# Performance work log

Measured on AMD Instinct MI355X. Metric: run time of the kernel, lower is better.

The kernel has to match this reference:

```python
import jax, jax.numpy as jnp
import numpy as np

N_NODES = 100000
N_EDGES = 1600000
D_IN = 256
N_HEADS = 4
D_OUT = 32
NEG_SLOPE = 0.2


def setup_inputs() -> dict:
    key = jax.random.key(0)
    k1, k2, k3, k4, k5, k6 = jax.random.split(key, 6)
    x = jax.random.normal(k1, (N_NODES, D_IN), dtype=jnp.float32)
    fc_w = jax.random.normal(k2, (N_HEADS * D_OUT, D_IN), dtype=jnp.float32) * (1.0 / np.sqrt(D_IN))
    attn_l = jax.random.normal(k3, (N_HEADS, D_OUT), dtype=jnp.float32) * 0.1
    attn_r = jax.random.normal(k4, (N_HEADS, D_OUT), dtype=jnp.float32) * 0.1
    src = jax.random.randint(k5, (N_EDGES,), 0, N_NODES, dtype=jnp.int64)
    dst = jax.random.randint(k6, (N_EDGES,), 0, N_NODES, dtype=jnp.int64)
    return {"x": x, "fc_w": fc_w, "attn_l": attn_l, "attn_r": attn_r, "src": src, "dst": dst}


def reference(x, fc_w, attn_l, attn_r, src, dst):
    N = x.shape[0]
    H, F = attn_l.shape
    # Linear projection: ft = fc(x) viewed as [N, H, F]
    ft = (x @ fc_w.T).reshape(N, H, F)
    # Per-node attention logits: el = <ft, a_l>, er = <ft, a_r>  -> [N, H]
    el = jnp.einsum("nhf,hf->nh", ft, attn_l)
    er = jnp.einsum("nhf,hf->nh", ft, attn_r)
    # Edge scores: e = leaky_relu(el[src] + er[dst])  -> [E, H]
    e = el[src] + er[dst]
    e = jnp.where(e > 0, e, NEG_SLOPE * e)
    # Segment (per-destination-node) softmax over incoming edges
    m = jax.ops.segment_max(e, dst, num_segments=N)  # [N, H]
    ex = jnp.exp(e - m[dst])                          # [E, H]
    denom = jax.ops.segment_sum(ex, dst, num_segments=N)  # [N, H]
    a = ex / denom[dst]                               # [E, H]
    # Weighted scatter-sum aggregation: out[n] = sum_{e: dst=n} a_e * ft[src_e]
    out = jax.ops.segment_sum(ft[src] * a[:, :, None], dst, num_segments=N)  # [N, H, F]
    return out
```

## Files before the change

### kernel.cpp

```cpp
#include <hip/hip_runtime.h>
#include <math.h>

#define N_NODES 100000
#define N_EDGES 1600000
#define D_IN 256
#define N_HEADS 4
#define D_OUT 32
#define D_HID 128
#define NEG_SLOPE 0.2f

#define BUCKET_SHIFT 8
#define BUCKET_NODES 256
#define NB ((N_NODES + BUCKET_NODES - 1) / BUCKET_NODES)
#define CAP 6144
#define TILE 2048
#define EPT 8
#define N_TILES ((N_EDGES + TILE - 1) / TILE)

typedef __attribute__((ext_vector_type(8))) short bf16x8;
typedef __attribute__((ext_vector_type(4))) float f32x4;

static __device__ __forceinline__ unsigned cvt2(float lo, float hi) {
  unsigned r;
  asm("v_cvt_pk_bf16_f32 %0, %1, %2" : "=v"(r) : "v"(lo), "v"(hi));
  return r;
}
static __device__ __forceinline__ float bfu_lo(unsigned u) {
  union { unsigned u; float f; } c; c.u = u << 16; return c.f;
}
static __device__ __forceinline__ float bfu_hi(unsigned u) {
  union { unsigned u; float f; } c; c.u = u & 0xFFFF0000u; return c.f;
}

#define LDA 40
__global__ __launch_bounds__(256) void k_gemm(const float* __restrict__ x,
                                              const float* __restrict__ w,
                                              const float* __restrict__ al,
                                              const float* __restrict__ ar,
                                              unsigned short* __restrict__ ftb,
                                              float* __restrict__ el,
                                              float* __restrict__ er) {
  __shared__ short As[128 * LDA];
  __shared__ short Bs[128 * LDA];
  int t = threadIdx.x;
  int wave = t >> 6, lane = t & 63;
  int quad = lane >> 4, l16 = lane & 15;
  int rowBase = blockIdx.x * 128;
  int wm = (wave >> 1) * 64, wn = (wave & 1) * 64;
  f32x4 acc[4][4];
  #pragma unroll
  for (int mt = 0; mt < 4; ++mt)
    #pragma unroll
    for (int nt = 0; nt < 4; ++nt) {
      acc[mt][nt][0] = 0.f; acc[mt][nt][1] = 0.f;
      acc[mt][nt][2] = 0.f; acc[mt][nt][3] = 0.f;
    }

  for (int kb = 0; kb < D_IN; kb += 32) {
    #pragma unroll
    for (int p = 0; p < 4; ++p) {
      int idx = p * 256 + t;
      int r = idx >> 3;
      int kq = (idx & 7) * 4;
      int row = rowBase + r;
      float4 v = make_float4(0.f, 0.f, 0.f, 0.f);
      if (row < N_NODES) v = *(const float4*)&x[(size_t)row * D_IN + kb + kq];
      unsigned* d = (unsigned*)&As[r * LDA + kq];
      d[0] = cvt2(v.x, v.y);
      d[1] = cvt2(v.z, v.w);
    }
    #pragma unroll
    for (int p = 0; p < 4; ++p) {
      int idx = p * 256 + t;
      int r = idx >> 3;
      int kq = (idx & 7) * 4;
      float4 v = *(const float4*)&w[(size_t)r * D_IN + kb + kq];
      unsigned* d = (unsigned*)&Bs[r * LDA + kq];
      d[0] = cvt2(v.x, v.y);
      d[1] = cvt2(v.z, v.w);
    }
    __syncthreads();
    bf16x8 af[4], bfr[4];
    #pragma unroll
    for (int mt = 0; mt < 4; ++mt)
      af[mt] = *(const bf16x8*)&As[(wm + mt * 16 + l16) * LDA + quad * 8];
    #pragma unroll
    for (int nt = 0; nt < 4; ++nt)
      bfr[nt] = *(const bf16x8*)&Bs[(wn + nt * 16 + l16) * LDA + quad * 8];
    #pragma unroll
    for (int mt = 0; mt < 4; ++mt)
      #pragma unroll
      for (int nt = 0; nt < 4; ++nt)
        acc[mt][nt] = __builtin_amdgcn_mfma_f32_16x16x32_bf16(af[mt], bfr[nt], acc[mt][nt], 0, 0, 0);
    __syncthreads();
  }

  #pragma unroll
  for (int mt = 0; mt < 4; ++mt) {
    #pragma unroll
    for (int nt = 0; nt < 4; ++nt) {
      int col = wn + nt * 16 + l16;
      #pragma unroll
      for (int r = 0; r < 4; r += 2) {
        unsigned p = cvt2(acc[mt][nt][r], acc[mt][nt][r + 1]);
        int row = rowBase + wm + mt * 16 + quad * 4 + r;
        if (row < N_NODES)
          ftb[(size_t)row * D_HID + col] = (unsigned short)p;
        if (row + 1 < N_NODES)
          ftb[(size_t)(row + 1) * D_HID + col] = (unsigned short)(p >> 16);
      }
    }
  }

  float alf[4], arf[4];
  #pragma unroll
  for (int q = 0; q < 4; ++q) {
    alf[q] = al[wn + q * 16 + l16];
    arf[q] = ar[wn + q * 16 + l16];
  }
  int h0 = wn >> 5;
  #pragma unroll
  for (int mt = 0; mt < 4; ++mt) {
    #pragma unroll
    for (int r = 0; r < 4; ++r) {
      float sl0 = acc[mt][0][r] * alf[0] + acc[mt][1][r] * alf[1];
      float sl1 = acc[mt][2][r] * alf[2] + acc[mt][3][r] * alf[3];
      float sr0 = acc[mt][0][r] * arf[0] + acc[mt][1][r] * arf[1];
      float sr1 = acc[mt][2][r] * arf[2] + acc[mt][3][r] * arf[3];
      #pragma unroll
      for (int o = 1; o < 16; o <<= 1) {
        sl0 += __shfl_xor(sl0, o);
        sl1 += __shfl_xor(sl1, o);
        sr0 += __shfl_xor(sr0, o);
        sr1 += __shfl_xor(sr1, o);
      }
      int row = rowBase + wm + mt * 16 + quad * 4 + r;
      if (l16 == 0 && row < N_NODES) {
        *(float2*)&el[row * 4 + h0] = make_float2(sl0, sl1);
        *(float2*)&er[row * 4 + h0] = make_float2(sr0, sr1);
      }
    }
  }
}

__global__ __launch_bounds__(256) void k_bucket(const int* __restrict__ src,
                                                const int* __restrict__ dst,
                                                int* __restrict__ gfill,
                                                unsigned* __restrict__ pairs,
                                                int* __restrict__ offs) {
  __shared__ int bcnt[NB];
  __shared__ int brsv[NB];
  __shared__ int brank[NB];
  int t = threadIdx.x;
  if (blockIdx.x == 0 && t == 0) offs[N_NODES] = N_EDGES;
  for (int tile = blockIdx.x; tile < N_TILES; tile += gridDim.x) {
    int e0 = tile * TILE + t * EPT;
    for (int i = t; i < NB; i += 256) { bcnt[i] = 0; brank[i] = 0; }
    __syncthreads();
    int ds[EPT], ss[EPT];
    if (e0 + EPT <= N_EDGES) {
      *(int4*)&ds[0] = *(const int4*)&dst[e0];
      *(int4*)&ds[4] = *(const int4*)&dst[e0 + 4];
      *(int4*)&ss[0] = *(const int4*)&src[e0];
      *(int4*)&ss[4] = *(const int4*)&src[e0 + 4];
    } else {
      #pragma unroll
      for (int k = 0; k < EPT; ++k) {
        int e = e0 + k;
        ds[k] = (e < N_EDGES) ? dst[e] : -1;
        ss[k] = (e < N_EDGES) ? src[e] : 0;
      }
    }
    #pragma unroll
    for (int k = 0; k < EPT; ++k)
      if (ds[k] >= 0) atomicAdd(&bcnt[ds[k] >> BUCKET_SHIFT], 1);
    __syncthreads();
    for (int i = t; i < NB; i += 256) {
      int c = bcnt[i];
      brsv[i] = (c > 0) ? atomicAdd(&gfill[i], c) : 0;
    }
    __syncthreads();
    #pragma unroll
    for (int k = 0; k < EPT; ++k) {
      if (ds[k] >= 0) {
        int b = ds[k] >> BUCKET_SHIFT;
        int r = brsv[b] + atomicAdd(&brank[b], 1);
        if (r < CAP)
          pairs[(size_t)b * CAP + r] =
              ((unsigned)ss[k] << 8) | (unsigned)(ds[k] & (BUCKET_NODES - 1));
      }
    }
    __syncthreads();
  }
}

__global__ __launch_bounds__(512) void k_localsort(const unsigned* __restrict__ pairs,
                                                   const int* __restrict__ gfill,
                                                   int* __restrict__ offs,
                                                   int* __restrict__ ssrc) {
  __shared__ int cnt_l[256];
  __shared__ int ss[256];
  __shared__ int cur_l[256];
  __shared__ int redsum[8];
  __shared__ int s_base;
  int b = blockIdx.x, t = threadIdx.x;
  {
    int v = (t < NB && t < b) ? gfill[t] : 0;
    #pragma unroll
    for (int o = 32; o > 0; o >>= 1) v += __shfl_xor(v, o);
    if ((t & 63) == 0) redsum[t >> 6] = v;
  }
  if (t < 256) cnt_l[t] = 0;
  __syncthreads();
  if (t == 0) {
    int s = 0;
    #pragma unroll
    for (int i = 0; i < 8; ++i) s += redsum[i];
    s_base = s;
  }
  int E = min(gfill[b], CAP);
  const unsigned* pb = &pairs[(size_t)b * CAP];
  __syncthreads();
  int base = s_base;
  for (int i = t; i < E; i += 512)
    atomicAdd(&cnt_l[pb[i] & (BUCKET_NODES - 1)], 1);
  __syncthreads();
  if (t < 256) ss[t] = cnt_l[t];
  __syncthreads();
  #pragma unroll
  for (int d = 1; d < 256; d <<= 1) {
    int u = (t < 256 && t >= d) ? ss[t - d] : 0;
    __syncthreads();
    if (t < 256) ss[t] += u;
    __syncthreads();
  }
  if (t < 256) {
    int pre = (t == 0) ? 0 : ss[t - 1];
    int node = b * BUCKET_NODES + t;
    if (node < N_NODES) offs[node] = base + pre;
    cur_l[t] = pre;
  }
  __syncthreads();
  for (int i = t; i < E; i += 512) {
    unsigned p = pb[i];
    int pos = atomicAdd(&cur_l[p & (BUCKET_NODES - 1)], 1);
    ssrc[base + pos] = (int)(p >> 8);
  }
}

#define AH_PAD 36
__global__ __launch_bounds__(256) void k_agg(const int* __restrict__ offs,
                                             const int* __restrict__ ssrc,
                                             const unsigned short* __restrict__ ftb,
                                             const float* __restrict__ el,
                                             const float* __restrict__ er,
                                             float* __restrict__ out) {
  __shared__ int   lds_s[4][2][32];
  __shared__ float lds_ah[4][2][4][AH_PAD];
  int wave = threadIdx.x >> 6;
  int lane = threadIdx.x & 63;
  int half = lane >> 5;
  int l32 = lane & 31;
  int n = blockIdx.x * 8 + wave * 2 + half;
  if (n >= N_NODES) return;
  int start = offs[n], end = offs[n + 1];
  int deg = end - start;

  int* sS = lds_s[wave][half];
  float (*sA)[AH_PAD] = lds_ah[wave][half];

  int c4 = l32 * 4;
  int hh = l32 >> 3;
  const unsigned short* fb = ftb + c4;
  float a0 = 0.f, a1 = 0.f, a2 = 0.f, a3 = 0.f;

  float4 er4 = *(const float4*)&er[n * 4];

  if (deg <= 32) {
    bool valid = l32 < deg;
    int s = valid ? ssrc[start + l32] : 0;
    float4 e4 = *(const float4*)&el[s * 4];
    float v[4] = {e4.x + er4.x, e4.y + er4.y, e4.z + er4.z, e4.w + er4.w};
    float m[4], ex[4], den[4];
    #pragma unroll
    for (int h = 0; h < 4; ++h) {
      v[h] = v[h] > 0.f ? v[h] : NEG_SLOPE * v[h];
      m[h] = valid ? v[h] : -INFINITY;
    }
    #pragma unroll
    for (int h = 0; h < 4; ++h)
      #pragma unroll
      for (int o = 16; o > 0; o >>= 1) m[h] = fmaxf(m[h], __shfl_xor(m[h], o));
    #pragma unroll
    for (int h = 0; h < 4; ++h) {
      ex[h] = valid ? __expf(v[h] - m[h]) : 0.f;
      den[h] = ex[h];
    }
    #pragma unroll
    for (int h = 0; h < 4; ++h)
      #pragma unroll
      for (int o = 16; o > 0; o >>= 1) den[h] += __shfl_xor(den[h], o);
    sS[l32] = s;
    #pragma unroll
    for (int h = 0; h < 4; ++h) sA[h][l32] = ex[h] / den[h];
    __builtin_amdgcn_wave_barrier();
    for (int j = 0; j < deg; j += 4) {
      int4   sv = *(const int4*)&sS[j];
      float4 av = *(const float4*)&sA[hh][j];
      uint2 uA = *(const uint2*)&fb[(size_t)sv.x * D_HID];
      uint2 uB = *(const uint2*)&fb[(size_t)sv.y * D_HID];
      uint2 uC = *(const uint2*)&fb[(size_t)sv.z * D_HID];
      uint2 uD = *(const uint2*)&fb[(size_t)sv.w * D_HID];
      a0 += av.x * bfu_lo(uA.x); a1 += av.x * bfu_hi(uA.x);
      a2 += av.x * bfu_lo(uA.y); a3 += av.x * bfu_hi(uA.y);
      a0 += av.y * bfu_lo(uB.x); a1 += av.y * bfu_hi(uB.x);
      a2 += av.y * bfu_lo(uB.y); a3 += av.y * bfu_hi(uB.y);
      a0 += av.z * bfu_lo(uC.x); a1 += av.z * bfu_hi(uC.x);
      a2 += av.z * bfu_lo(uC.y); a3 += av.z * bfu_hi(uC.y);
      a0 += av.w * bfu_lo(uD.x); a1 += av.w * bfu_hi(uD.x);
      a2 += av.w * bfu_lo(uD.y); a3 += av.w * bfu_hi(uD.y);
    }
  } else {
    float erh[4] = {er4.x, er4.y, er4.z, er4.w};
    float m[4] = {-INFINITY, -INFINITY, -INFINITY, -INFINITY};
    for (int c = start; c < end; c += 32) {
      int i = c + l32;
      bool valid = i < end;
      int s = valid ? ssrc[i] : 0;
      float4 e4 = *(const float4*)&el[s * 4];
      float ee[4] = {e4.x, e4.y, e4.z, e4.w};
      #pragma unroll
      for (int h = 0; h < 4; ++h) {
        float v = ee[h] + erh[h];
        v = v > 0.f ? v : NEG_SLOPE * v;
        m[h] = fmaxf(m[h], valid ? v : -INFINITY);
      }
    }
    #pragma unroll
    for (int h = 0; h < 4; ++h)
      #pragma unroll
      for (int o = 16; o > 0; o >>= 1) m[h] = fmaxf(m[h], __shfl_xor(m[h], o));
    float den[4] = {0.f, 0.f, 0.f, 0.f};
    for (int c = start; c < end; c += 32) {
      int i = c + l32;
      bool valid = i < end;
      int s = valid ? ssrc[i] : 0;
      float4 e4 = *(const float4*)&el[s * 4];
      float ee[4] = {e4.x, e4.y, e4.z, e4.w};
      #pragma unroll
      for (int h = 0; h < 4; ++h) {
        float v = ee[h] + erh[h];
        v = v > 0.f ? v : NEG_SLOPE * v;
        den[h] += valid ? __expf(v - m[h]) : 0.f;
      }
    }
    #pragma unroll
    for (int h = 0; h < 4; ++h)
      #pragma unroll
      for (int o = 16; o > 0; o >>= 1) den[h] += __shfl_xor(den[h], o);
    float invd[4];
    #pragma unroll
    for (int h = 0; h < 4; ++h) invd[h] = 1.f / den[h];
    for (int c = start; c < end; c += 32) {
      int i = c + l32;
      bool valid = i < end;
      int s = valid ? ssrc[i] : 0;
      float4 e4 = *(const float4*)&el[s * 4];
      float ee[4] = {e4.x, e4.y, e4.z, e4.w};
      float av[4];
      #pragma unroll
      for (int h = 0; h < 4; ++h) {
        float v = ee[h] + erh[h];
        v = v > 0.f ? v : NEG_SLOPE * v;
        av[h] = valid ? __expf(v - m[h]) * invd[h] : 0.f;
      }
      __builtin_amdgcn_wave_barrier();
      sS[l32] = s;
      #pragma unroll
      for (int h = 0; h < 4; ++h) sA[h][l32] = av[h];
      __builtin_amdgcn_wave_barrier();
      int cnt = min(32, end - c);
      for (int j = 0; j < cnt; j += 4) {
        int4   sv = *(const int4*)&sS[j];
        float4 aw = *(const float4*)&sA[hh][j];
        uint2 uA = *(const uint2*)&fb[(size_t)sv.x * D_HID];
        uint2 uB = *(const uint2*)&fb[(size_t)sv.y * D_HID];
        uint2 uC = *(const uint2*)&fb[(size_t)sv.z * D_HID];
        uint2 uD = *(const uint2*)&fb[(size_t)sv.w * D_HID];
        a0 += aw.x * bfu_lo(uA.x); a1 += aw.x * bfu_hi(uA.x);
        a2 += aw.x * bfu_lo(uA.y); a3 += aw.x * bfu_hi(uA.y);
        a0 += aw.y * bfu_lo(uB.x); a1 += aw.y * bfu_hi(uB.x);
        a2 += aw.y * bfu_lo(uB.y); a3 += aw.y * bfu_hi(uB.y);
        a0 += aw.z * bfu_lo(uC.x); a1 += aw.z * bfu_hi(uC.x);
        a2 += aw.z * bfu_lo(uC.y); a3 += aw.z * bfu_hi(uC.y);
        a0 += aw.w * bfu_lo(uD.x); a1 += aw.w * bfu_hi(uD.x);
        a2 += aw.w * bfu_lo(uD.y); a3 += aw.w * bfu_hi(uD.y);
      }
    }
  }
  *(float4*)&out[(size_t)n * D_HID + c4] = make_float4(a0, a1, a2, a3);
}

extern "C" void kernel_launch(void* const* d_in, const int* in_sizes, int n_in,
                              void* d_out, int out_size, void* d_ws, size_t ws_size,
                              hipStream_t stream) {
  const float* x      = (const float*)d_in[0];
  const float* fc_w   = (const float*)d_in[1];
  const float* attn_l = (const float*)d_in[2];
  const float* attn_r = (const float*)d_in[3];
  const int*   src    = (const int*)d_in[4];
  const int*   dst    = (const int*)d_in[5];
  float* out = (float*)d_out;

  char* wsp = (char*)d_ws;
  size_t off = 0;
  auto alloc = [&](size_t bytes) {
    void* p = wsp + off;
    off = (off + bytes + 255) & ~(size_t)255;
    return p;
  };
  unsigned short* ftb = (unsigned short*)alloc((size_t)N_NODES * D_HID * 2);
  float* el     = (float*)alloc((size_t)N_NODES * 4 * 4);
  float* er     = (float*)alloc((size_t)N_NODES * 4 * 4);
  int*   offs   = (int*)alloc((size_t)(N_NODES + 1) * 4);
  int*   ssrc   = (int*)alloc((size_t)N_EDGES * 4);
  int*   gfill  = (int*)alloc((size_t)NB * 4);
  unsigned* pairs = (unsigned*)alloc((size_t)NB * CAP * 4);

  hipMemsetAsync(gfill, 0, (size_t)NB * 4, stream);
  k_gemm<<<(N_NODES + 127) / 128, 256, 0, stream>>>(x, fc_w, attn_l, attn_r, ftb, el, er);
  k_bucket<<<N_TILES, 256, 0, stream>>>(src, dst, gfill, pairs, offs);
  k_localsort<<<NB, 512, 0, stream>>>(pairs, gfill, offs, ssrc);
  k_agg<<<(N_NODES + 7) / 8, 256, 0, stream>>>(offs, ssrc, ftb, el, er, out);
}
```

Measured before the change: 331.4 us.

## Drop LDS staging in projection GEMM; load operands directly into registers

Result: slower. 351.8 us (+6.1%).

```diff
diff --git a/kernel.cpp b/kernel.cpp
--- a/kernel.cpp
+++ b/kernel.cpp
@@ -32,78 +32,101 @@
   union { unsigned u; float f; } c; c.u = u & 0xFFFF0000u; return c.f;
 }
 
-#define LDA 40
+__global__ __launch_bounds__(256) void k_wcvt(const float* __restrict__ w,
+                                              unsigned short* __restrict__ wb) {
+  int i = blockIdx.x * 256 + threadIdx.x;
+  if (i < (D_HID * D_IN) / 4) {
+    float4 v = ((const float4*)w)[i];
+    ((uint2*)wb)[i] = make_uint2(cvt2(v.x, v.y), cvt2(v.z, v.w));
+  }
+}
+
 __global__ __launch_bounds__(256) void k_gemm(const float* __restrict__ x,
-                                              const float* __restrict__ w,
+                                              const unsigned short* __restrict__ wb,
                                               const float* __restrict__ al,
                                               const float* __restrict__ ar,
                                               unsigned short* __restrict__ ftb,
                                               float* __restrict__ el,
                                               float* __restrict__ er) {
-  __shared__ short As[128 * LDA];
-  __shared__ short Bs[128 * LDA];
   int t = threadIdx.x;
   int wave = t >> 6, lane = t & 63;
   int quad = lane >> 4, l16 = lane & 15;
-  int rowBase = blockIdx.x * 128;
-  int wm = (wave >> 1) * 64, wn = (wave & 1) * 64;
-  f32x4 acc[4][4];
+  int rowBase = blockIdx.x * 256 + wave * 64;
+
+  f32x4 acc[4][8];
   #pragma unroll
   for (int mt = 0; mt < 4; ++mt)
     #pragma unroll
-    for (int nt = 0; nt < 4; ++nt) {
+    for (int nt = 0; nt < 8; ++nt) {
       acc[mt][nt][0] = 0.f; acc[mt][nt][1] = 0.f;
       acc[mt][nt][2] = 0.f; acc[mt][nt][3] = 0.f;
     }
 
+  const float* xr[4];
+  bool rv[4];
+  #pragma unroll
+  for (int mt = 0; mt < 4; ++mt) {
+    int row = rowBase + mt * 16 + l16;
+    rv[mt] = row < N_NODES;
+    xr[mt] = x + (size_t)(rv[mt] ? row : 0) * D_IN + quad * 8;
+  }
+  const unsigned short* wr = wb + l16 * D_IN + quad * 8;
+  const float4 z4 = make_float4(0.f, 0.f, 0.f, 0.f);
+
+  float4 xb[4][2];
+  #pragma unroll
+  for (int mt = 0; mt < 4; ++mt) {
+    xb[mt][0] = rv[mt] ? *(const float4*)(xr[mt]) : z4;
+    xb[mt][1] = rv[mt] ? *(const float4*)(xr[mt] + 4) : z4;
+  }
+
+  #pragma unroll
   for (int kb = 0; kb < D_IN; kb += 32) {
-    #pragma unroll
-    for (int p = 0; p < 4; ++p) {
-      int idx = p * 256 + t;
-      int r = idx >> 3;
-      int kq = (idx & 7) * 4;
-      int row = rowBase + r;
-      float4 v = make_float4(0.f, 0.f, 0.f, 0.f);
-      if (row < N_NODES) v = *(const float4*)&x[(size_t)row * D_IN + kb + kq];
-      unsigned* d = (unsigned*)&As[r * LDA + kq];
-      d[0] = cvt2(v.x, v.y);
-      d[1] = cvt2(v.z, v.w);
-    }
-    #pragma unroll
-    for (int p = 0; p < 4; ++p) {
-      int idx = p * 256 + t;
-      int r = idx >> 3;
-      int kq = (idx & 7) * 4;
-      float4 v = *(const float4*)&w[(size_t)r * D_IN + kb + kq];
-      unsigned* d = (unsigned*)&Bs[r * LDA + kq];
-      d[0] = cvt2(v.x, v.y);
-      d[1] = cvt2(v.z, v.w);
-    }
-    __syncthreads();
-    bf16x8 af[4], bfr[4];
+    float4 xn[4][2];
+    if (kb + 32 < D_IN) {
+      #pragma unroll
+      for (int mt = 0; mt < 4; ++mt) {
+        xn[mt][0] = rv[mt] ? *(const float4*)(xr[mt] + kb + 32) : z4;
+        xn[mt][1] = rv[mt] ? *(const float4*)(xr[mt] + kb + 36) : z4;
+      }
+    }
+    bf16x8 bfr[8];
+    #pragma unroll
+    for (int nt = 0; nt < 8; ++nt)
+      bfr[nt] = *(const bf16x8*)(wr + nt * 16 * D_IN + kb);
+    bf16x8 af[4];
+    #pragma unroll
+    for (int mt = 0; mt < 4; ++mt) {
+      union { unsigned u[4]; bf16x8 v; } c;
+      c.u[0] = cvt2(xb[mt][0].x, xb[mt][0].y);
+      c.u[1] = cvt2(xb[mt][0].z, xb[mt][0].w);
+      c.u[2] = cvt2(xb[mt][1].x, xb[mt][1].y);
+      c.u[3] = cvt2(xb[mt][1].z, xb[mt][1].w);
+      af[mt] = c.v;
+    }
     #pragma unroll
     for (int mt = 0; mt < 4; ++mt)
-      af[mt] = *(const bf16x8*)&As[(wm + mt * 16 + l16) * LDA + quad * 8];
-    #pragma unroll
-    for (int nt = 0; nt < 4; ++nt)
-      bfr[nt] = *(const bf16x8*)&Bs[(wn + nt * 16 + l16) * LDA + quad * 8];
-    #pragma unroll
-    for (int mt = 0; mt < 4; ++mt)
-      #pragma unroll
-      for (int nt = 0; nt < 4; ++nt)
+      #pragma unroll
+      for (int nt = 0; nt < 8; ++nt)
         acc[mt][nt] = __builtin_amdgcn_mfma_f32_16x16x32_bf16(af[mt], bfr[nt], acc[mt][nt], 0, 0, 0);
-    __syncthreads();
+    if (kb + 32 < D_IN) {
+      #pragma unroll
+      for (int mt = 0; mt < 4; ++mt) {
+        xb[mt][0] = xn[mt][0];
+        xb[mt][1] = xn[mt][1];
+      }
+    }
   }
 
   #pragma unroll
   for (int mt = 0; mt < 4; ++mt) {
     #pragma unroll
-    for (int nt = 0; nt < 4; ++nt) {
-      int col = wn + nt * 16 + l16;
+    for (int nt = 0; nt < 8; ++nt) {
+      int col = nt * 16 + l16;
       #pragma unroll
       for (int r = 0; r < 4; r += 2) {
         unsigned p = cvt2(acc[mt][nt][r], acc[mt][nt][r + 1]);
-        int row = rowBase + wm + mt * 16 + quad * 4 + r;
+        int row = rowBase + mt * 16 + quad * 4 + r;
         if (row < N_NODES)
           ftb[(size_t)row * D_HID + col] = (unsigned short)p;
         if (row + 1 < N_NODES)
@@ -112,32 +135,34 @@
     }
   }
 
-  float alf[4], arf[4];
-  #pragma unroll
-  for (int q = 0; q < 4; ++q) {
-    alf[q] = al[wn + q * 16 + l16];
-    arf[q] = ar[wn + q * 16 + l16];
-  }
-  int h0 = wn >> 5;
+  float alf[8], arf[8];
+  #pragma unroll
+  for (int nt = 0; nt < 8; ++nt) {
+    alf[nt] = al[nt * 16 + l16];
+    arf[nt] = ar[nt * 16 + l16];
+  }
   #pragma unroll
   for (int mt = 0; mt < 4; ++mt) {
     #pragma unroll
     for (int r = 0; r < 4; ++r) {
-      float sl0 = acc[mt][0][r] * alf[0] + acc[mt][1][r] * alf[1];
-      float sl1 = acc[mt][2][r] * alf[2] + acc[mt][3][r] * alf[3];
-      float sr0 = acc[mt][0][r] * arf[0] + acc[mt][1][r] * arf[1];
-      float sr1 = acc[mt][2][r] * arf[2] + acc[mt][3][r] * arf[3];
+      int row = rowBase + mt * 16 + quad * 4 + r;
+      float sl[4], sr[4];
+      #pragma unroll
+      for (int h = 0; h < 4; ++h) {
+        sl[h] = acc[mt][2 * h][r] * alf[2 * h] + acc[mt][2 * h + 1][r] * alf[2 * h + 1];
+        sr[h] = acc[mt][2 * h][r] * arf[2 * h] + acc[mt][2 * h + 1][r] * arf[2 * h + 1];
+      }
       #pragma unroll
       for (int o = 1; o < 16; o <<= 1) {
-        sl0 += __shfl_xor(sl0, o);
-        sl1 += __shfl_xor(sl1, o);
-        sr0 += __shfl_xor(sr0, o);
-        sr1 += __shfl_xor(sr1, o);
-      }
-      int row = rowBase + wm + mt * 16 + quad * 4 + r;
+        #pragma unroll
+        for (int h = 0; h < 4; ++h) {
+          sl[h] += __shfl_xor(sl[h], o);
+          sr[h] += __shfl_xor(sr[h], o);
+        }
+      }
       if (l16 == 0 && row < N_NODES) {
-        *(float2*)&el[row * 4 + h0] = make_float2(sl0, sl1);
-        *(float2*)&er[row * 4 + h0] = make_float2(sr0, sr1);
+        *(float4*)&el[row * 4] = make_float4(sl[0], sl[1], sl[2], sl[3]);
+        *(float4*)&er[row * 4] = make_float4(sr[0], sr[1], sr[2], sr[3]);
       }
     }
   }
@@ -420,6 +445,7 @@
     return p;
   };
   unsigned short* ftb = (unsigned short*)alloc((size_t)N_NODES * D_HID * 2);
+  unsigned short* wb  = (unsigned short*)alloc((size_t)D_HID * D_IN * 2);
   float* el     = (float*)alloc((size_t)N_NODES * 4 * 4);
   float* er     = (float*)alloc((size_t)N_NODES * 4 * 4);
   int*   offs   = (int*)alloc((size_t)(N_NODES + 1) * 4);
@@ -428,7 +454,8 @@
   unsigned* pairs = (unsigned*)alloc((size_t)NB * CAP * 4);
 
   hipMemsetAsync(gfill, 0, (size_t)NB * 4, stream);
-  k_gemm<<<(N_NODES + 127) / 128, 256, 0, stream>>>(x, fc_w, attn_l, attn_r, ftb, el, er);
+  k_wcvt<<<(D_HID * D_IN / 4 + 255) / 256, 256, 0, stream>>>(fc_w, wb);
+  k_gemm<<<(N_NODES + 255) / 256, 256, 0, stream>>>(x, wb, attn_l, attn_r, ftb, el, er);
   k_bucket<<<N_TILES, 256, 0, stream>>>(src, dst, gfill, pairs, offs);
   k_localsort<<<NB, 512, 0, stream>>>(pairs, gfill, offs, ssrc);
   k_agg<<<(N_NODES + 7) / 8, 256, 0, stream>>>(offs, ssrc, ftb, el, er, out);
```
